# Optimization experiments

Measured on AMD Instinct MI355X. Metric: run time of the kernel, lower is better.

## Reference

```python
import jax, jax.numpy as jnp
import numpy as np

B, S, DM, H = 8, 512, 1024, 16
D = DM // H            # head_dim = 64
NFEAT = 4              # len(feature_types)
N_DIST = 2 * 512 - 1   # max_utt_num*2-1 = 1023
N_DISC = 16 + 1        # len(DISCOURSE_RELATIONS)+1
N_COOC = 5 + 1


def setup_inputs() -> dict:
    key = jax.random.key(0)
    ks = jax.random.split(key, 24)
    inp = {}
    inp["query"] = jax.random.normal(ks[0], (B, S, DM), jnp.float32)
    inp["key"] = jax.random.normal(ks[1], (B, S, DM), jnp.float32)
    inp["value"] = jax.random.normal(ks[2], (B, S, DM), jnp.float32)
    inp["distance_adj"] = jax.random.randint(ks[3], (B, S, S), 0, N_DIST).astype(jnp.int32)
    inp["speaker_adj"] = jax.random.uniform(ks[4], (B, S, S), jnp.float32)
    inp["discourse_adj"] = jax.random.randint(ks[5], (B, S, S), 0, N_DISC).astype(jnp.int32)
    inp["cooccurrence_adj"] = jax.random.randint(ks[6], (B, S, S), 0, N_COOC).astype(jnp.int32)
    inp["mask"] = jnp.ones((B, 1, 1, S), jnp.int32)
    w = lambda k, shape: jax.random.normal(k, shape, jnp.float32) * 0.02
    inp["Wq"] = w(ks[7], (DM, DM)); inp["bq"] = jnp.zeros((DM,), jnp.float32)
    inp["Wk"] = w(ks[8], (DM, DM)); inp["bk"] = jnp.zeros((DM,), jnp.float32)
    inp["Wv"] = w(ks[9], (DM, DM)); inp["bv"] = jnp.zeros((DM,), jnp.float32)
    inp["Wo"] = w(ks[10], (DM, DM)); inp["bo"] = jnp.zeros((DM,), jnp.float32)
    inp["dist_embed"] = w(ks[11], (N_DIST, 1))
    inp["disc_embed"] = w(ks[12], (N_DISC, 1)).at[0].set(0.0)  # padding_idx=0
    inp["cooc_embed"] = w(ks[13], (N_COOC, 1)).at[0].set(0.0)  # padding_idx=0
    inp["fcw"] = w(ks[14], (H, NFEAT))       # per-head 1x1 conv weights
    inp["fcb"] = jnp.zeros((H,), jnp.float32)
    inp["cw"] = w(ks[15], (2,))              # combine conv weights
    inp["cb"] = jnp.zeros((), jnp.float32)
    return inp


def reference(query, key, value, distance_adj, speaker_adj, discourse_adj,
              cooccurrence_adj, mask, Wq, bq, Wk, bk, Wv, bv, Wo, bo,
              dist_embed, disc_embed, cooc_embed, fcw, fcb, cw, cb):
    scale = jnp.asarray(D ** 0.5, query.dtype)
    # Linear projections, split heads -> [B, H, S, D]
    split = lambda x: x.reshape(B, S, H, D).transpose(0, 2, 1, 3)
    Q = split(query @ Wq.T + bq)
    K = split(key @ Wk.T + bk)
    V = split(value @ Wv.T + bv)
    energy = jnp.einsum('bhqd,bhkd->bhqk', Q, K) / scale  # [B,H,S,S]
    # Adjacency feature maps in feature_types order: distance, speaker, discourse, cooccurrence
    dist = dist_embed[distance_adj, 0]
    disc = disc_embed[discourse_adj, 0] * (discourse_adj != 0)
    cooc = cooc_embed[cooccurrence_adj, 0] * (cooccurrence_adj != 0)
    feature_map = jnp.stack([dist, speaker_adj, disc, cooc], axis=1)  # [B,4,S,S]
    # Per-head 1x1 conv over the 4 feature channels + relu
    feat = jax.nn.relu(jnp.einsum('hc,bcij->bhij', fcw, feature_map)
                       + fcb[None, :, None, None])       # [B,H,S,S]
    # Combine conv (1x1, 2 channels -> 1) + relu
    energy = jax.nn.relu(cw[0] * energy + cw[1] * feat + cb)
    energy = jnp.where(mask == 0, -jnp.inf, energy)
    attention = jax.nn.softmax(energy, axis=-1)           # [B,H,S,S]
    x = jnp.einsum('bhqk,bhkd->bhqd', attention, V)       # dropout p=0 (eval)
    x = x.transpose(0, 2, 1, 3).reshape(B, S, DM)
    x = x @ Wo.T + bo
    return x, attention
```

## Files before the change

### kernel.cpp

```cpp
#include <hip/hip_runtime.h>

using short8 = __attribute__((ext_vector_type(8))) short;
using f32x4  = __attribute__((ext_vector_type(4))) float;

__device__ __forceinline__ unsigned short f2bf(float x) {
    union { float f; unsigned u; } v; v.f = x;
    unsigned u = v.u;
    unsigned r = (u + 0x7fffu + ((u >> 16) & 1u)) >> 16;
    return (unsigned short)r;
}
__device__ __forceinline__ float bf2f(unsigned short h) {
    union { unsigned u; float f; } v; v.u = ((unsigned)h) << 16;
    return v.f;
}

__device__ __forceinline__ void async16(const void* g, void* l) {
    __builtin_amdgcn_global_load_lds(
        (const __attribute__((address_space(1))) void*)g,
        (__attribute__((address_space(3))) void*)l, 16, 0, 0);
}

__global__ __launch_bounds__(256) void cvt_qkv(
    const float* __restrict__ q, const float* __restrict__ k, const float* __restrict__ v,
    unsigned short* __restrict__ dst)
{
    int z = blockIdx.z;
    const float* src = (z == 0) ? q : ((z == 1) ? k : v);
    unsigned short* o = dst + (size_t)z * 4194304;
    size_t i = ((size_t)blockIdx.x * 256 + threadIdx.x) * 8;
    float4 a = *(const float4*)(src + i);
    float4 b = *(const float4*)(src + i + 4);
    ushort4 lo, hi;
    lo.x = f2bf(a.x); lo.y = f2bf(a.y); lo.z = f2bf(a.z); lo.w = f2bf(a.w);
    hi.x = f2bf(b.x); hi.y = f2bf(b.y); hi.z = f2bf(b.z); hi.w = f2bf(b.w);
    *(ushort4*)(o + i) = lo;
    *(ushort4*)(o + i + 4) = hi;
}

__global__ __launch_bounds__(256) void cvt_w(
    const float* __restrict__ wq, const float* __restrict__ wk,
    const float* __restrict__ wv, const float* __restrict__ wo,
    unsigned short* __restrict__ dst)
{
    int z = blockIdx.z;
    const float* src = (z == 0) ? wq : ((z == 1) ? wk : ((z == 2) ? wv : wo));
    unsigned short* o = dst + (size_t)z * 1048576;
    size_t i = ((size_t)blockIdx.x * 256 + threadIdx.x) * 8;
    float4 a = *(const float4*)(src + i);
    float4 b = *(const float4*)(src + i + 4);
    ushort4 lo, hi;
    lo.x = f2bf(a.x); lo.y = f2bf(a.y); lo.z = f2bf(a.z); lo.w = f2bf(a.w);
    hi.x = f2bf(b.x); hi.y = f2bf(b.y); hi.z = f2bf(b.z); hi.w = f2bf(b.w);
    *(ushort4*)(o + i) = lo;
    *(ushort4*)(o + i + 4) = hi;
}

__global__ __launch_bounds__(256) void feat_kernel(
    const int* __restrict__ dist_adj, const float* __restrict__ spk,
    const int* __restrict__ disc_adj, const int* __restrict__ cooc_adj,
    const float* __restrict__ dist_emb, const float* __restrict__ disc_emb,
    const float* __restrict__ cooc_emb, const float* __restrict__ fcw,
    const float* __restrict__ fcb, const float* __restrict__ cw,
    unsigned short* __restrict__ G)
{
    __shared__ float s_dist[1023];
    __shared__ float s_disc[17];
    __shared__ float s_cooc[6];
    __shared__ float s_fcw[64];
    __shared__ float s_fcb[16];
    int tid = threadIdx.x;
    for (int i = tid; i < 1023; i += 256) s_dist[i] = dist_emb[i];
    if (tid < 17) s_disc[tid] = disc_emb[tid];
    if (tid < 6)  s_cooc[tid] = cooc_emb[tid];
    if (tid < 64) s_fcw[tid]  = fcw[tid];
    if (tid < 16) s_fcb[tid]  = fcb[tid];
    __syncthreads();
    float cw1 = cw[1];

    int bx = blockIdx.x;
    int k  = (bx & 1) * 256 + tid;
    int qq = (bx >> 1) & 127;
    int b  = bx >> 8;

    size_t abase = ((size_t)b * 512 + qq * 4) * 512 + k;
    float f0[4], f1[4], f2[4], f3[4];
#pragma unroll
    for (int r = 0; r < 4; ++r) {
        size_t a = abase + (size_t)r * 512;
        int dd = dist_adj[a];
        f1[r]  = spk[a];
        int dc = disc_adj[a];
        int cc = cooc_adj[a];
        f0[r] = s_dist[dd];
        f2[r] = dc ? s_disc[dc] : 0.f;
        f3[r] = cc ? s_cooc[cc] : 0.f;
    }

    size_t gq = ((size_t)b * 16 * 128 + qq) * 512 + k;
#pragma unroll
    for (int h = 0; h < 16; ++h) {
        float w0 = s_fcw[h*4+0], w1 = s_fcw[h*4+1], w2 = s_fcw[h*4+2], w3 = s_fcw[h*4+3];
        float bb = s_fcb[h];
        ushort4 o;
        o.x = f2bf(fmaxf(w0*f0[0] + w1*f1[0] + w2*f2[0] + w3*f3[0] + bb, 0.f) * cw1);
        o.y = f2bf(fmaxf(w0*f0[1] + w1*f1[1] + w2*f2[1] + w3*f3[1] + bb, 0.f) * cw1);
        o.z = f2bf(fmaxf(w0*f0[2] + w1*f1[2] + w2*f2[2] + w3*f3[2] + bb, 0.f) * cw1);
        o.w = f2bf(fmaxf(w0*f0[3] + w1*f1[3] + w2*f2[3] + w3*f3[3] + bb, 0.f) * cw1);
        *(ushort4*)(G + (gq + (size_t)h * 65536) * 4) = o;
    }
}

template<int OMODE>
__device__ __forceinline__ void gemm_bf16_body(
    const unsigned short* __restrict__ A, const unsigned short* __restrict__ W,
    const float* __restrict__ bias, void* __restrict__ outp, int m0, int n0)
{
    __shared__ __align__(16) unsigned short As[128 * 32];
    __shared__ __align__(16) unsigned short Bs[128 * 32];
    int tid = threadIdx.x;
    int lane = tid & 63, wid = tid >> 6;
    int wx = wid & 1, wy = wid >> 1;
    int lanelo = lane & 15, hi8 = (lane >> 4) * 8;
    int rowc = lane >> 2;
    int colc = (lane & 3) * 8;

    f32x4 acc[4][4];
#pragma unroll
    for (int i = 0; i < 4; ++i)
#pragma unroll
        for (int j = 0; j < 4; ++j) {
            acc[i][j][0] = 0.f; acc[i][j][1] = 0.f; acc[i][j][2] = 0.f; acc[i][j][3] = 0.f;
        }

    for (int kk = 0; kk < 32; ++kk) {
        int k0 = kk * 32;
        __syncthreads();
#pragma unroll
        for (int p = 0; p < 2; ++p) {
            int c = 2 * wid + p;
            int row = c * 16 + rowc;
            async16(A + (size_t)(m0 + row) * 1024 + k0 + colc, As + c * 512);
        }
#pragma unroll
        for (int p = 0; p < 2; ++p) {
            int c = 2 * wid + p;
            int row = c * 16 + rowc;
            async16(W + (size_t)(n0 + row) * 1024 + k0 + colc, Bs + c * 512);
        }
        __syncthreads();

        short8 af[4], bfr[4];
#pragma unroll
        for (int i = 0; i < 4; ++i)
            af[i] = *(const short8*)(As + (wy*64 + i*16 + lanelo) * 32 + hi8);
#pragma unroll
        for (int j = 0; j < 4; ++j)
            bfr[j] = *(const short8*)(Bs + (wx*64 + j*16 + lanelo) * 32 + hi8);
#pragma unroll
        for (int i = 0; i < 4; ++i)
#pragma unroll
            for (int j = 0; j < 4; ++j)
                acc[i][j] = __builtin_amdgcn_mfma_f32_16x16x32_bf16(af[i], bfr[j], acc[i][j], 0, 0, 0);
    }

    float bia[4];
#pragma unroll
    for (int j = 0; j < 4; ++j) bia[j] = bias[n0 + wx*64 + j*16 + lanelo];
#pragma unroll
    for (int i = 0; i < 4; ++i) {
        int mbase = m0 + wy*64 + i*16 + (lane >> 4) * 4;
#pragma unroll
        for (int j = 0; j < 4; ++j) {
            int n = n0 + wx*64 + j*16 + lanelo;
#pragma unroll
            for (int r = 0; r < 4; ++r) {
                int m = mbase + r;
                float val = acc[i][j][r] + bia[j];
                if (OMODE == 0) {
                    unsigned short* o = (unsigned short*)outp;
                    o[((size_t)((m >> 9) * 16 + (n >> 6)) * 512 + (m & 511)) * 64 + (n & 63)] = f2bf(val);
                } else {
                    float* o = (float*)outp;
                    o[(size_t)m * 1024 + n] = val;
                }
            }
        }
    }
}

__global__ __launch_bounds__(256) void gemm_qkv(
    const unsigned short* __restrict__ Abf, const unsigned short* __restrict__ Wbf,
    const float* __restrict__ bq, const float* __restrict__ bk, const float* __restrict__ bv,
    unsigned short* Qb, unsigned short* Kb, unsigned short* Vb)
{
    int z = blockIdx.z;
    const unsigned short* A = Abf + (size_t)z * 4194304;
    const unsigned short* W = Wbf + (size_t)z * 1048576;
    const float* bias = (z == 0) ? bq : ((z == 1) ? bk : bv);
    unsigned short* o = (z == 0) ? Qb : ((z == 1) ? Kb : Vb);
    gemm_bf16_body<0>(A, W, bias, o, blockIdx.x * 128, blockIdx.y * 128);
}

__global__ __launch_bounds__(256) void gemm_proj(
    const unsigned short* __restrict__ xh, const unsigned short* __restrict__ Wo,
    const float* __restrict__ bo, float* __restrict__ out)
{
    gemm_bf16_body<1>(xh, Wo, bo, out, blockIdx.x * 128, blockIdx.y * 128);
}

__global__ __launch_bounds__(256) void transpose_v(const unsigned short* __restrict__ Vb,
                                                   unsigned short* __restrict__ Vt)
{
    __shared__ __align__(16) unsigned short T[64][72];
    int tid = threadIdx.x;
    int s0 = blockIdx.x * 64;
    int bh = blockIdx.z * 16 + blockIdx.y;
#pragma unroll
    for (int p = 0; p < 2; ++p) {
        int c = p * 256 + tid;
        int row = c >> 3, kc = (c & 7) * 8;
        uint4 v = *(const uint4*)(Vb + ((size_t)bh * 512 + s0 + row) * 64 + kc);
        *(uint4*)&T[row][kc] = v;
    }
    __syncthreads();
#pragma unroll
    for (int p = 0; p < 2; ++p) {
        int c = p * 256 + tid;
        int d = c >> 3, sc = (c & 7) * 8;
        unsigned vv[4];
#pragma unroll
        for (int i = 0; i < 4; ++i) {
            unsigned lo = T[sc + 2*i][d];
            unsigned hi = T[sc + 2*i + 1][d];
            vv[i] = lo | (hi << 16);
        }
        uint4 o; o.x = vv[0]; o.y = vv[1]; o.z = vv[2]; o.w = vv[3];
        *(uint4*)(Vt + ((size_t)bh * 64 + d) * 512 + s0 + sc) = o;
    }
}

__global__ __launch_bounds__(256, 4) void attn_kernel(
    const unsigned short* __restrict__ Qb, const unsigned short* __restrict__ Kb,
    const unsigned short* __restrict__ Vt, const unsigned short* __restrict__ G,
    const int* __restrict__ mask, const float* __restrict__ cw,
    const float* __restrict__ cb, float* __restrict__ attn_out,
    unsigned short* __restrict__ xh)
{
    __shared__ __align__(16) char smem[39936];
    unsigned short (*Qs)[72]     = (unsigned short (*)[72])smem;
    unsigned short (*Ks)[72]     = (unsigned short (*)[72])(smem + 9216);
    float          (*PT)[16][68] = (float (*)[16][68])smem;
    unsigned short (*Vs)[40]     = (unsigned short (*)[40])(smem + 27648);
    unsigned short (*Ps)[16][40] = (unsigned short (*)[16][40])(smem + 32768);
    int* s_mask = (int*)(smem + 37888);

    int tid = threadIdx.x;
    int lane = tid & 63, w = tid >> 6;
    int lanelo = lane & 15, hi8 = (lane >> 4) * 8;
    int hi2 = lane >> 4;

    int lin = blockIdx.x;
    int xcd = lin & 7;
    int s   = lin >> 3;
    int bh  = xcd * 16 + (s >> 3);
    int qt  = s & 7;
    int b   = bh >> 4, h = bh & 15;

    float qs  = cw[0] * 0.125f;
    float cbv = cb[0];

    s_mask[tid]       = mask[b * 512 + tid];
    s_mask[tid + 256] = mask[b * 512 + tid + 256];
#pragma unroll
    for (int p = 0; p < 2; ++p) {
        int c = p * 256 + tid;
        int row = c >> 3, kc = (c & 7) * 8;
        uint4 v = *(const uint4*)(Qb + ((size_t)bh * 512 + qt * 64 + row) * 64 + kc);
        *(uint4*)&Qs[row][kc] = v;
    }
    __syncthreads();

    short8 aq[2];
    aq[0] = *(const short8*)&Qs[w * 16 + lanelo][hi8];
    aq[1] = *(const short8*)&Qs[w * 16 + lanelo][32 + hi8];
    int qrow = qt * 64 + w * 16 + hi2 * 4;
    int qq   = qt * 16 + w * 4 + hi2;
    const unsigned short* gbase = G + ((size_t)bh * 128 + qq) * 2048;

    float P[32][4];
#pragma unroll 1
    for (int kt = 0; kt < 4; ++kt) {
        ushort4 g[8];
#pragma unroll
        for (int j = 0; j < 8; ++j)
            g[j] = *(const ushort4*)(gbase + (kt * 8 + j) * 64 + lanelo * 4);
        __syncthreads();
#pragma unroll
        for (int p = 0; p < 4; ++p) {
            int c = p * 256 + tid;
            int row = c >> 3, kc = (c & 7) * 8;
            uint4 v = *(const uint4*)(Kb + ((size_t)bh * 512 + kt * 128 + row) * 64 + kc);
            *(uint4*)&Ks[row][kc] = v;
        }
        __syncthreads();
#pragma unroll
        for (int j = 0; j < 8; ++j) {
            short8 b0 = *(const short8*)&Ks[j * 16 + lanelo][hi8];
            short8 b1 = *(const short8*)&Ks[j * 16 + lanelo][32 + hi8];
            f32x4 acc; acc[0] = 0.f; acc[1] = 0.f; acc[2] = 0.f; acc[3] = 0.f;
            acc = __builtin_amdgcn_mfma_f32_16x16x32_bf16(aq[0], b0, acc, 0, 0, 0);
            acc = __builtin_amdgcn_mfma_f32_16x16x32_bf16(aq[1], b1, acc, 0, 0, 0);
            int jj = kt * 8 + j;
            int kcol = jj * 16 + lanelo;
            int mk = s_mask[kcol];
            float gf[4] = { bf2f(g[j].x), bf2f(g[j].y), bf2f(g[j].z), bf2f(g[j].w) };
#pragma unroll
            for (int r = 0; r < 4; ++r) {
                float e = qs * acc[r] + gf[r] + cbv;
                e = fmaxf(e, 0.f);
                P[jj][r] = mk ? __expf(e) : 0.f;
            }
        }
    }
    __syncthreads();

    float inv[4];
#pragma unroll
    for (int r = 0; r < 4; ++r) {
        float s0 = 0.f;
#pragma unroll
        for (int jj = 0; jj < 32; ++jj) s0 += P[jj][r];
        s0 += __shfl_xor(s0, 1, 64);
        s0 += __shfl_xor(s0, 2, 64);
        s0 += __shfl_xor(s0, 4, 64);
        s0 += __shfl_xor(s0, 8, 64);
        inv[r] = 1.0f / s0;
    }

    {
        float* PTw = &PT[w][0][0];
        float* op  = attn_out + ((size_t)bh * 512 + qt * 64 + w * 16) * 512;
#pragma unroll
        for (int c = 0; c < 8; ++c) {
#pragma unroll
            for (int jc = 0; jc < 4; ++jc) {
                int jj = c * 4 + jc;
#pragma unroll
                for (int r = 0; r < 4; ++r)
                    PTw[(hi2 * 4 + r) * 68 + jc * 16 + lanelo] = P[jj][r] * inv[r];
            }
            asm volatile("s_waitcnt lgkmcnt(0)" ::: "memory");
#pragma unroll
            for (int p = 0; p < 4; ++p) {
                int row = p * 4 + hi2;
                float4 v4 = *(const float4*)&PTw[row * 68 + lanelo * 4];
                *(float4*)(op + (size_t)row * 512 + c * 64 + lanelo * 4) = v4;
            }
            asm volatile("" ::: "memory");
        }
    }

    f32x4 xacc[4];
#pragma unroll
    for (int jf = 0; jf < 4; ++jf) { xacc[jf][0]=0.f; xacc[jf][1]=0.f; xacc[jf][2]=0.f; xacc[jf][3]=0.f; }
#pragma unroll 1
    for (int ks = 0; ks < 16; ++ks) {
        __syncthreads();
        {
            int d = tid >> 2, kc = (tid & 3) * 8;
            uint4 v = *(const uint4*)(Vt + ((size_t)bh * 64 + d) * 512 + ks * 32 + kc);
            *(uint4*)&Vs[d][kc] = v;
        }
#pragma unroll
        for (int ff = 0; ff < 2; ++ff) {
            int f = ks * 2 + ff;
#pragma unroll
            for (int r = 0; r < 4; ++r)
                Ps[w][hi2 * 4 + r][ff * 16 + lanelo] = f2bf(P[f][r]);
        }
        __syncthreads();
        short8 ap8 = *(const short8*)&Ps[w][lanelo][hi8];
#pragma unroll
        for (int jf = 0; jf < 4; ++jf) {
            short8 bv = *(const short8*)&Vs[jf * 16 + lanelo][hi8];
            xacc[jf] = __builtin_amdgcn_mfma_f32_16x16x32_bf16(ap8, bv, xacc[jf], 0, 0, 0);
        }
    }

    {
        unsigned short* XT = (unsigned short*)(PT + w);
        asm volatile("" ::: "memory");
#pragma unroll
        for (int jf = 0; jf < 4; ++jf)
#pragma unroll
            for (int r = 0; r < 4; ++r)
                XT[(hi2 * 4 + r) * 68 + jf * 16 + lanelo] = f2bf(xacc[jf][r] * inv[r]);
        asm volatile("s_waitcnt lgkmcnt(0)" ::: "memory");
        unsigned short* xp = xh + ((size_t)b * 512 + qt * 64 + w * 16) * 1024 + h * 64;
#pragma unroll
        for (int p = 0; p < 4; ++p) {
            int row = p * 4 + hi2;
            ushort4 v = *(const ushort4*)&XT[row * 68 + lanelo * 4];
            *(ushort4*)(xp + (size_t)row * 1024 + lanelo * 4) = v;
        }
    }
}

extern "C" void kernel_launch(void* const* d_in, const int* in_sizes, int n_in,
                              void* d_out, int out_size, void* d_ws, size_t ws_size,
                              hipStream_t stream) {
    (void)in_sizes; (void)n_in; (void)out_size; (void)ws_size;
    const float* query    = (const float*)d_in[0];
    const float* key      = (const float*)d_in[1];
    const float* value    = (const float*)d_in[2];
    const int*   dist_adj = (const int*)d_in[3];
    const float* spk      = (const float*)d_in[4];
    const int*   disc_adj = (const int*)d_in[5];
    const int*   cooc_adj = (const int*)d_in[6];
    const int*   maskp    = (const int*)d_in[7];
    const float* Wq = (const float*)d_in[8];  const float* bq = (const float*)d_in[9];
    const float* Wk = (const float*)d_in[10]; const float* bk = (const float*)d_in[11];
    const float* Wv = (const float*)d_in[12]; const float* bv = (const float*)d_in[13];
    const float* Wo = (const float*)d_in[14]; const float* bo = (const float*)d_in[15];
    const float* dist_emb = (const float*)d_in[16];
    const float* disc_emb = (const float*)d_in[17];
    const float* cooc_emb = (const float*)d_in[18];
    const float* fcw = (const float*)d_in[19];
    const float* fcb = (const float*)d_in[20];
    const float* cw  = (const float*)d_in[21];
    const float* cbp = (const float*)d_in[22];

    char* w = (char*)d_ws;
    unsigned short* Qb  = (unsigned short*)(w);
    unsigned short* Kb  = (unsigned short*)(w + 8388608);
    unsigned short* Vb  = (unsigned short*)(w + 16777216);
    unsigned short* Vt  = (unsigned short*)(w + 25165824);
    unsigned short* xh  = (unsigned short*)(w + 33554432);
    unsigned short* G   = (unsigned short*)(w + 41943040);
    unsigned short* Abf = G;
    unsigned short* Wbf = (unsigned short*)(w + 109051904);

    float* out_x    = (float*)d_out;
    float* attn_out = ((float*)d_out) + 4194304;

    cvt_qkv<<<dim3(2048, 1, 3), 256, 0, stream>>>(query, key, value, Abf);
    cvt_w<<<dim3(512, 1, 4), 256, 0, stream>>>(Wq, Wk, Wv, Wo, Wbf);
    gemm_qkv<<<dim3(32, 8, 3), 256, 0, stream>>>(Abf, Wbf, bq, bk, bv, Qb, Kb, Vb);
    transpose_v<<<dim3(8, 16, 8), 256, 0, stream>>>(Vb, Vt);
    feat_kernel<<<2048, 256, 0, stream>>>(dist_adj, spk, disc_adj, cooc_adj,
                                          dist_emb, disc_emb, cooc_emb, fcw, fcb, cw, G);
    attn_kernel<<<dim3(1024, 1, 1), 256, 0, stream>>>(Qb, Kb, Vt, G, maskp, cw, cbp,
                                                      attn_out, xh);
    gemm_proj<<<dim3(32, 8), 256, 0, stream>>>(xh, Wbf + 3145728, bo, out_x);
}
```

Before: 468.0 us.

## Store attention probabilities directly with nontemporal stores and fully unroll loops

Removes the LDS transpose staging for the attention-probability and output writes and stores straight from registers, using nontemporal stores for the large attention matrix and nontemporal loads for the feature tensor. The K-tile and PV loops are fully unrolled, and the shared-memory aliasing is replaced by separate arrays. Occupancy is lowered to 2 blocks per CU to allow more registers. The direct stores are 4-byte, strided across rows, so they are less coalesced than the previous float4 row writes, which risks lower store efficiency.

```diff
diff --git a/kernel.cpp b/kernel.cpp
--- a/kernel.cpp
+++ b/kernel.cpp
@@ -2,6 +2,7 @@
 
 using short8 = __attribute__((ext_vector_type(8))) short;
 using f32x4  = __attribute__((ext_vector_type(4))) float;
+typedef unsigned short u16x4 __attribute__((ext_vector_type(4)));
 
 __device__ __forceinline__ unsigned short f2bf(float x) {
     union { float f; unsigned u; } v; v.f = x;
@@ -239,20 +240,18 @@
     }
 }
 
-__global__ __launch_bounds__(256, 4) void attn_kernel(
+__global__ __launch_bounds__(256, 2) void attn_kernel(
     const unsigned short* __restrict__ Qb, const unsigned short* __restrict__ Kb,
     const unsigned short* __restrict__ Vt, const unsigned short* __restrict__ G,
     const int* __restrict__ mask, const float* __restrict__ cw,
     const float* __restrict__ cb, float* __restrict__ attn_out,
     unsigned short* __restrict__ xh)
 {
-    __shared__ __align__(16) char smem[39936];
-    unsigned short (*Qs)[72]     = (unsigned short (*)[72])smem;
-    unsigned short (*Ks)[72]     = (unsigned short (*)[72])(smem + 9216);
-    float          (*PT)[16][68] = (float (*)[16][68])smem;
-    unsigned short (*Vs)[40]     = (unsigned short (*)[40])(smem + 27648);
-    unsigned short (*Ps)[16][40] = (unsigned short (*)[16][40])(smem + 32768);
-    int* s_mask = (int*)(smem + 37888);
+    __shared__ __align__(16) unsigned short Qs[64][72];
+    __shared__ __align__(16) unsigned short Ks[128][72];
+    __shared__ __align__(16) unsigned short Vs[64][40];
+    __shared__ __align__(16) unsigned short Ps[4][16][40];
+    __shared__ int s_mask[512];
 
     int tid = threadIdx.x;
     int lane = tid & 63, w = tid >> 6;
@@ -288,12 +287,13 @@
     const unsigned short* gbase = G + ((size_t)bh * 128 + qq) * 2048;
 
     float P[32][4];
-#pragma unroll 1
+#pragma unroll
     for (int kt = 0; kt < 4; ++kt) {
-        ushort4 g[8];
+        u16x4 g[8];
 #pragma unroll
         for (int j = 0; j < 8; ++j)
-            g[j] = *(const ushort4*)(gbase + (kt * 8 + j) * 64 + lanelo * 4);
+            g[j] = __builtin_nontemporal_load(
+                (const u16x4*)(gbase + (kt * 8 + j) * 64 + lanelo * 4));
         __syncthreads();
 #pragma unroll
         for (int p = 0; p < 4; ++p) {
@@ -313,7 +313,8 @@
             int jj = kt * 8 + j;
             int kcol = jj * 16 + lanelo;
             int mk = s_mask[kcol];
-            float gf[4] = { bf2f(g[j].x), bf2f(g[j].y), bf2f(g[j].z), bf2f(g[j].w) };
+            float gf[4] = { bf2f((unsigned short)g[j][0]), bf2f((unsigned short)g[j][1]),
+                            bf2f((unsigned short)g[j][2]), bf2f((unsigned short)g[j][3]) };
 #pragma unroll
             for (int r = 0; r < 4; ++r) {
                 float e = qs * acc[r] + gf[r] + cbv;
@@ -322,7 +323,6 @@
             }
         }
     }
-    __syncthreads();
 
     float inv[4];
 #pragma unroll
@@ -338,32 +338,19 @@
     }
 
     {
-        float* PTw = &PT[w][0][0];
-        float* op  = attn_out + ((size_t)bh * 512 + qt * 64 + w * 16) * 512;
-#pragma unroll
-        for (int c = 0; c < 8; ++c) {
-#pragma unroll
-            for (int jc = 0; jc < 4; ++jc) {
-                int jj = c * 4 + jc;
-#pragma unroll
-                for (int r = 0; r < 4; ++r)
-                    PTw[(hi2 * 4 + r) * 68 + jc * 16 + lanelo] = P[jj][r] * inv[r];
-            }
-            asm volatile("s_waitcnt lgkmcnt(0)" ::: "memory");
-#pragma unroll
-            for (int p = 0; p < 4; ++p) {
-                int row = p * 4 + hi2;
-                float4 v4 = *(const float4*)&PTw[row * 68 + lanelo * 4];
-                *(float4*)(op + (size_t)row * 512 + c * 64 + lanelo * 4) = v4;
-            }
-            asm volatile("" ::: "memory");
-        }
+        float* ap = attn_out + ((size_t)bh * 512 + qrow) * 512 + lanelo;
+#pragma unroll
+        for (int jj = 0; jj < 32; ++jj)
+#pragma unroll
+            for (int r = 0; r < 4; ++r)
+                __builtin_nontemporal_store(P[jj][r] * inv[r],
+                                            ap + (size_t)r * 512 + jj * 16);
     }
 
     f32x4 xacc[4];
 #pragma unroll
     for (int jf = 0; jf < 4; ++jf) { xacc[jf][0]=0.f; xacc[jf][1]=0.f; xacc[jf][2]=0.f; xacc[jf][3]=0.f; }
-#pragma unroll 1
+#pragma unroll
     for (int ks = 0; ks < 16; ++ks) {
         __syncthreads();
         {
@@ -387,21 +374,13 @@
         }
     }
 
-    {
-        unsigned short* XT = (unsigned short*)(PT + w);
-        asm volatile("" ::: "memory");
-#pragma unroll
-        for (int jf = 0; jf < 4; ++jf)
-#pragma unroll
-            for (int r = 0; r < 4; ++r)
-                XT[(hi2 * 4 + r) * 68 + jf * 16 + lanelo] = f2bf(xacc[jf][r] * inv[r]);
-        asm volatile("s_waitcnt lgkmcnt(0)" ::: "memory");
-        unsigned short* xp = xh + ((size_t)b * 512 + qt * 64 + w * 16) * 1024 + h * 64;
-#pragma unroll
-        for (int p = 0; p < 4; ++p) {
-            int row = p * 4 + hi2;
-            ushort4 v = *(const ushort4*)&XT[row * 68 + lanelo * 4];
-            *(ushort4*)(xp + (size_t)row * 1024 + lanelo * 4) = v;
+#pragma unroll
+    for (int jf = 0; jf < 4; ++jf) {
+        int d = jf * 16 + lanelo;
+#pragma unroll
+        for (int r = 0; r < 4; ++r) {
+            float val = xacc[jf][r] * inv[r];
+            xh[((size_t)b * 512 + qrow + r) * 1024 + h * 64 + d] = f2bf(val);
         }
     }
 }
```

Result: faster. 381.5 us (-18.5%).
